# Kernel optimization log

Hardware: AMD Instinct MI355X
Metric: run time of the kernel (lower is better)

## Reference

```python
import jax, jax.numpy as jnp
import numpy as np

B, T, D = 4, 2048, 768
H, HD = 8, 96          # n_heads, head_dim
NB = HD // 24          # number of 24-dim Leech blocks per head
NEG_INF = -1e30


def _leech_kernel_24():
    # QR of the bidiagonal/circulant base matrix, as in generate_leech_kernel
    base = np.zeros((24, 24), dtype=np.float32)
    for i in range(23):
        base[i, i] = 2.0
        base[i, i + 1] = 2.0
    base[23, 23] = 2.0
    base[23, 0] = -2.0
    q, _ = np.linalg.qr(base)
    return jnp.asarray(q, dtype=jnp.float32)


def setup_inputs() -> dict:
    key = jax.random.key(0)
    k1, k2, k3 = jax.random.split(key, 3)
    x = jax.random.normal(k1, (B, T, D), dtype=jnp.float32)
    w_qkv = jax.random.normal(k2, (3 * D, D), dtype=jnp.float32) * (D ** -0.5)
    w_out = jax.random.normal(k3, (D, D), dtype=jnp.float32) * (D ** -0.5)
    kernel = _leech_kernel_24()
    return {"x": x, "w_qkv": w_qkv, "w_out": w_out, "kernel": kernel}


def reference(x, w_qkv, w_out, kernel):
    Bx, Tx, Dx = x.shape
    scale = HD ** -0.5
    # qkv projection (bias=False)
    qkv = jnp.einsum('btd,ed->bte', x, w_qkv)            # [B,T,3D]
    qkv = qkv.reshape(Bx, Tx, 3, H, HD).transpose(2, 0, 3, 1, 4)  # [3,B,H,T,HD]
    q, k, v = qkv[0], qkv[1], qkv[2]
    # per-24-block orthogonal Leech rotation on q and k
    q = jnp.einsum('bhtni,ij->bhtnj', q.reshape(Bx, H, Tx, NB, 24), kernel)
    k = jnp.einsum('bhtni,ij->bhtnj', k.reshape(Bx, H, Tx, NB, 24), kernel)
    q = q.reshape(Bx, H, Tx, HD)
    k = k.reshape(Bx, H, Tx, HD)
    # causal attention (manual softmax; dropout inactive in eval)
    scores = jnp.einsum('bhqd,bhkd->bhqk', q, k) * scale
    causal = jnp.tril(jnp.ones((Tx, Tx), dtype=bool))
    scores = jnp.where(causal[None, None], scores, NEG_INF)
    attn = jax.nn.softmax(scores, axis=-1)
    out = jnp.einsum('bhqk,bhkd->bhqd', attn, v)          # [B,H,T,HD]
    out = out.transpose(0, 2, 1, 3).reshape(Bx, Tx, Dx)
    return jnp.einsum('btd,ed->bte', out, w_out)
```

## Files before the change

kernel.cpp:

```cpp
#include <hip/hip_runtime.h>
#include <cstdint>
#include <cstddef>

#define Bq 4
#define T 2048
#define Dm 768
#define H 8
#define HD 96
#define BH 32
#define QEL ((size_t)BH*T*HD)
#define KEL ((size_t)BH*T*128)
#define PSTRIDE 98304
#define QS 0.14724703336f
#define KVB 64
#define M0 12.0f

typedef unsigned int u32;
typedef unsigned long long u64;
typedef _Float16 f16x8 __attribute__((ext_vector_type(8)));
typedef _Float16 f16x4 __attribute__((ext_vector_type(4)));
typedef float f32x4 __attribute__((ext_vector_type(4)));

__global__ __launch_bounds__(256)
void cvt_fused(const float* __restrict__ x, const float* __restrict__ wq,
               const float* __restrict__ wo, _Float16* __restrict__ xh,
               _Float16* __restrict__ wqh, _Float16* __restrict__ woh)
{
    const int tid  = threadIdx.x;
    const int lane = tid & 63;
    const int gw   = (blockIdx.x * 256 + tid) >> 6;
    const int kc   = gw % 96;
    const int grp  = gw / 96;

    const float* in;
    _Float16* out;
    int row;
    if (grp < 128)      { in = x;  out = xh;  row = grp * 64 + lane; }
    else if (grp < 164) { in = wq; out = wqh; row = (grp - 128) * 64 + lane; }
    else                { in = wo; out = woh; row = (grp - 164) * 64 + lane; }

    const float4 a = *reinterpret_cast<const float4*>(in + (size_t)row * 768 + kc * 8);
    const float4 b = *reinterpret_cast<const float4*>(in + (size_t)row * 768 + kc * 8 + 4);
    f16x8 h;
    h[0] = (_Float16)a.x; h[1] = (_Float16)a.y; h[2] = (_Float16)a.z; h[3] = (_Float16)a.w;
    h[4] = (_Float16)b.x; h[5] = (_Float16)b.y; h[6] = (_Float16)b.z; h[7] = (_Float16)b.w;
    *reinterpret_cast<f16x8*>(
        out + (size_t)(row >> 7) * PSTRIDE + (size_t)kc * 1024 + (row & 127) * 8) = h;
}

template <bool SCATTER>
__global__ __launch_bounds__(256)
void gemm_mfma(const _Float16* __restrict__ At, const _Float16* __restrict__ Bt,
               _Float16* __restrict__ qb, _Float16* __restrict__ kpd,
               _Float16* __restrict__ vtb, float* __restrict__ C,
               int N, int nx)
{
    constexpr int NSTEP = Dm / 32;
    __shared__ _Float16 As[2][4 * 128 * 8];
    __shared__ _Float16 Bs[2][4 * 128 * 8];

    const int tid  = threadIdx.x;
    const int lane = tid & 63;
    const int wid  = tid >> 6;
    const int li   = lane & 15;
    const int lg   = lane >> 4;
    const int wr   = wid >> 1;
    const int wc   = wid & 1;

    const int qch = gridDim.x >> 3;
    const int id  = (blockIdx.x & 7) * qch + (blockIdx.x >> 3);
    const int m0  = (id / nx) * 128;
    const int n0  = (id % nx) * 128;

    const _Float16* baseA = At + (size_t)(m0 >> 7) * PSTRIDE;
    const _Float16* baseB = Bt + (size_t)(n0 >> 7) * PSTRIDE;

    f32x4 acc[4][4];
#pragma unroll
    for (int i = 0; i < 4; ++i)
#pragma unroll
        for (int j = 0; j < 4; ++j) acc[i][j] = (f32x4)0.f;

    auto STAGE = [&](int t, int b) {
        const _Float16* pa = baseA + (t << 12);
        const _Float16* pb = baseB + (t << 12);
#pragma unroll
        for (int i = 0; i < 2; ++i) {
            const int s = wid * 64 + i * 256;
            __builtin_amdgcn_global_load_lds(
                (const __attribute__((address_space(1))) void*)(pa + (size_t)(s + lane) * 8),
                (__attribute__((address_space(3))) void*)&As[b][s * 8], 16, 0, 0);
            __builtin_amdgcn_global_load_lds(
                (const __attribute__((address_space(1))) void*)(pb + (size_t)(s + lane) * 8),
                (__attribute__((address_space(3))) void*)&Bs[b][s * 8], 16, 0, 0);
        }
    };

    STAGE(0, 0);
    for (int t = 0; t < NSTEP; ++t) {
        const int p = t & 1;
        if (t + 1 < NSTEP) {
            STAGE(t + 1, p ^ 1);
            asm volatile("s_waitcnt vmcnt(4)" ::: "memory");
        } else {
            asm volatile("s_waitcnt vmcnt(0)" ::: "memory");
        }
        __builtin_amdgcn_s_barrier();

        f16x8 af[4], bf[4];
#pragma unroll
        for (int i = 0; i < 4; ++i)
            af[i] = *reinterpret_cast<const f16x8*>(
                &As[p][(lg * 128 + wr * 64 + i * 16 + li) * 8]);
#pragma unroll
        for (int j = 0; j < 4; ++j)
            bf[j] = *reinterpret_cast<const f16x8*>(
                &Bs[p][(lg * 128 + wc * 64 + j * 16 + li) * 8]);
#pragma unroll
        for (int i = 0; i < 4; ++i)
#pragma unroll
            for (int j = 0; j < 4; ++j)
                acc[i][j] = __builtin_amdgcn_mfma_f32_16x16x32_f16(
                    af[i], bf[j], acc[i][j], 0, 0, 0);

        asm volatile("s_waitcnt lgkmcnt(0)" ::: "memory");
        __builtin_amdgcn_s_barrier();
    }

#pragma unroll
    for (int i = 0; i < 4; ++i) {
#pragma unroll
        for (int r = 0; r < 4; ++r) {
            const int m = m0 + wr * 64 + i * 16 + lg * 4 + r;
            if (SCATTER) {
                const int b_ = m >> 11, t_ = m & 2047;
#pragma unroll
                for (int j = 0; j < 4; ++j) {
                    const int e = n0 + wc * 64 + j * 16 + li;
                    const int c = e / Dm;
                    const int rem = e - c * Dm;
                    const int h = rem / HD;
                    const int d = rem - h * HD;
                    const size_t bhx = (size_t)(b_ * H + h);
                    const float v = acc[i][j][r];
                    if (c == 0)
                        qb[(bhx * T + t_) * HD + d] = (_Float16)(v * QS);
                    else if (c == 1)
                        kpd[(bhx * T + t_) * 128 + d] = (_Float16)v;
                    else
                        vtb[(bhx * 96 + d) * T + t_] = (_Float16)v;
                }
            } else {
#pragma unroll
                for (int j = 0; j < 4; ++j) {
                    const int n = n0 + wc * 64 + j * 16 + li;
                    C[(size_t)m * N + n] = acc[i][j][r];
                }
            }
        }
    }
}

__global__ __launch_bounds__(256)
void attn_mfma(const _Float16* __restrict__ QG, const _Float16* __restrict__ KG,
               const _Float16* __restrict__ VtG, _Float16* __restrict__ aoh)
{
    __shared__ __align__(16) _Float16 Klds[2][64 * 128];
    __shared__ __align__(16) _Float16 Vlds[2][112 * 64];
    __shared__ __align__(16) _Float16 Pl[4][16][72];

    const int tid  = threadIdx.x;
    const int lane = tid & 63;
    const int wid  = tid >> 6;
    const int lg   = lane >> 4;
    const int li   = lane & 15;

    const int bh = blockIdx.x & 31;
    const int i  = blockIdx.x >> 5;
    const int qt0 = i, qt1 = 31 - i;

    {
        const u32 one2 = 0x3C003C00u;
        u32* vp0 = reinterpret_cast<u32*>(&Vlds[0][96 * 64]);
        u32* vp1 = reinterpret_cast<u32*>(&Vlds[1][96 * 64]);
#pragma unroll
        for (int k = tid; k < 512; k += 256) {
            const u32 v = (k < 32) ? one2 : 0u;
            vp0[k] = v; vp1[k] = v;
        }
    }
    __syncthreads();

    f16x8 qf0[3], qf1[3];
    {
        const _Float16* qr0 = QG + ((size_t)bh * T + qt0 * 64 + wid * 16 + li) * HD;
        const _Float16* qr1 = QG + ((size_t)bh * T + qt1 * 64 + wid * 16 + li) * HD;
#pragma unroll
        for (int ch = 0; ch < 3; ++ch) {
            qf0[ch] = *reinterpret_cast<const f16x8*>(qr0 + ch * 32 + lg * 8);
            qf1[ch] = *reinterpret_cast<const f16x8*>(qr1 + ch * 32 + lg * 8);
        }
    }

    const int swz = (li & 7) << 3;
    int kofs[4][3], vofs[7][2];
#pragma unroll
    for (int kt = 0; kt < 4; ++kt)
#pragma unroll
        for (int ch = 0; ch < 3; ++ch)
            kofs[kt][ch] = (kt * 16 + li) * 128 + ((ch * 32 + lg * 8) ^ swz);
#pragma unroll
    for (int dt = 0; dt < 7; ++dt)
#pragma unroll
        for (int pc = 0; pc < 2; ++pc)
            vofs[dt][pc] = (dt * 16 + li) * 64 + ((pc * 32 + lg * 8) ^ swz);

    const int rK = lane >> 4;
    const int cK = (lane & 15) * 8;
    const int rV = lane >> 3;
    const int cV = (lane & 7) * 8;
    auto STAGE = [&](int kb, int b) {
#pragma unroll
        for (int ii = 0; ii < 4; ++ii) {
            const int r  = wid * 16 + ii * 4 + rK;
            const int c0 = cK ^ (((ii * 4 + rK) & 7) << 3);
            const _Float16* src = KG + ((size_t)(bh * T + kb + r)) * 128 + c0;
            __builtin_amdgcn_global_load_lds(
                (const __attribute__((address_space(1))) void*)src,
                (__attribute__((address_space(3))) void*)&Klds[b][(wid * 16 + ii * 4) * 128],
                16, 0, 0);
        }
#pragma unroll
        for (int jj = 0; jj < 3; ++jj) {
            const int r  = wid * 24 + jj * 8 + rV;
            const int c0 = cV ^ (rV << 3);
            const _Float16* src = VtG + ((size_t)(bh * 96 + r)) * T + kb + c0;
            __builtin_amdgcn_global_load_lds(
                (const __attribute__((address_space(1))) void*)src,
                (__attribute__((address_space(3))) void*)&Vlds[b][(wid * 24 + jj * 8) * 64],
                16, 0, 0);
        }
    };

    f32x4 acc0[7], acc1[7];
#pragma unroll
    for (int dt = 0; dt < 7; ++dt) { acc0[dt] = (f32x4)0.f; acc1[dt] = (f32x4)0.f; }

    auto ROUND_FULL = [&](const f16x8 (&qf)[3], f32x4 (&acc)[7],
                          int p, int nextkb) {
        STAGE(nextkb, p ^ 1);
        asm volatile("s_waitcnt vmcnt(7)" ::: "memory");
        __builtin_amdgcn_s_barrier();

        const _Float16* Kb = &Klds[p][0];
        const _Float16* Vb = &Vlds[p][0];

        f16x8 kf[4][3];
#pragma unroll
        for (int kt = 0; kt < 4; ++kt)
#pragma unroll
            for (int ch = 0; ch < 3; ++ch)
                kf[kt][ch] = *reinterpret_cast<const f16x8*>(Kb + kofs[kt][ch]);

        f32x4 st[4];
        __builtin_amdgcn_s_setprio(1);
#pragma unroll
        for (int kt = 0; kt < 4; ++kt) {
            st[kt] = (f32x4)(-M0);
#pragma unroll
            for (int ch = 0; ch < 3; ++ch)
                st[kt] = __builtin_amdgcn_mfma_f32_16x16x32_f16(
                    kf[kt][ch], qf[ch], st[kt], 0, 0, 0);
        }
        __builtin_amdgcn_s_setprio(0);

#pragma unroll
        for (int kt = 0; kt < 4; ++kt) {
            const auto a = __builtin_amdgcn_cvt_pkrtz(
                __builtin_amdgcn_exp2f(st[kt][0]),
                __builtin_amdgcn_exp2f(st[kt][1]));
            const auto b = __builtin_amdgcn_cvt_pkrtz(
                __builtin_amdgcn_exp2f(st[kt][2]),
                __builtin_amdgcn_exp2f(st[kt][3]));
            const u64 w = (u64)__builtin_bit_cast(u32, a) |
                          ((u64)__builtin_bit_cast(u32, b) << 32);
            *reinterpret_cast<u64*>(&Pl[wid][li][kt * 16 + lg * 4]) = w;
        }

#pragma unroll
        for (int pc = 0; pc < 2; ++pc) {
            const f16x8 pf = *reinterpret_cast<const f16x8*>(
                &Pl[wid][li][pc * 32 + lg * 8]);
            __builtin_amdgcn_s_setprio(1);
#pragma unroll
            for (int dt = 0; dt < 7; ++dt) {
                const f16x8 vf = *reinterpret_cast<const f16x8*>(Vb + vofs[dt][pc]);
                acc[dt] = __builtin_amdgcn_mfma_f32_16x16x32_f16(
                    pf, vf, acc[dt], 0, 0, 0);
            }
            __builtin_amdgcn_s_setprio(0);
        }

        asm volatile("s_waitcnt lgkmcnt(0)" ::: "memory");
        __builtin_amdgcn_s_barrier();
    };

    auto ROUND_DIAG = [&](int kb, int q0w, const f16x8 (&qf)[3], f32x4 (&acc)[7],
                          int p, int nextkb, bool has_next) {
        if (has_next) {
            STAGE(nextkb, p ^ 1);
            asm volatile("s_waitcnt vmcnt(7)" ::: "memory");
        } else {
            asm volatile("s_waitcnt vmcnt(0)" ::: "memory");
        }
        __builtin_amdgcn_s_barrier();

        const _Float16* Kb = &Klds[p][0];
        const _Float16* Vb = &Vlds[p][0];
        const int nkt = min(4, ((q0w + 15 - kb) >> 4) + 1);

        f16x8 kf[4][3];
#pragma unroll
        for (int kt = 0; kt < 4; ++kt)
            if (kt < nkt) {
#pragma unroll
                for (int ch = 0; ch < 3; ++ch)
                    kf[kt][ch] = *reinterpret_cast<const f16x8*>(Kb + kofs[kt][ch]);
            }

        f32x4 st[4];
        __builtin_amdgcn_s_setprio(1);
#pragma unroll
        for (int kt = 0; kt < 4; ++kt) {
            st[kt] = (f32x4)(-M0);
            if (kt < nkt) {
#pragma unroll
                for (int ch = 0; ch < 3; ++ch)
                    st[kt] = __builtin_amdgcn_mfma_f32_16x16x32_f16(
                        kf[kt][ch], qf[ch], st[kt], 0, 0, 0);
            }
        }
        __builtin_amdgcn_s_setprio(0);

        const int qg = q0w + li;
#pragma unroll
        for (int kt = 0; kt < 4; ++kt)
            if (kt < nkt && kb + kt * 16 + 15 > q0w) {
#pragma unroll
                for (int rr = 0; rr < 4; ++rr) {
                    const int kg = kb + kt * 16 + lg * 4 + rr;
                    if (kg > qg) st[kt][rr] = -1e30f;
                }
            }

#pragma unroll
        for (int kt = 0; kt < 4; ++kt)
            if (kt < nkt) {
                const auto a = __builtin_amdgcn_cvt_pkrtz(
                    __builtin_amdgcn_exp2f(st[kt][0]),
                    __builtin_amdgcn_exp2f(st[kt][1]));
                const auto b = __builtin_amdgcn_cvt_pkrtz(
                    __builtin_amdgcn_exp2f(st[kt][2]),
                    __builtin_amdgcn_exp2f(st[kt][3]));
                const u64 w = (u64)__builtin_bit_cast(u32, a) |
                              ((u64)__builtin_bit_cast(u32, b) << 32);
                *reinterpret_cast<u64*>(&Pl[wid][li][kt * 16 + lg * 4]) = w;
            }
        if (nkt & 1)
            *reinterpret_cast<u64*>(&Pl[wid][li][nkt * 16 + lg * 4]) = 0ull;

        const int npc = (nkt + 1) >> 1;
#pragma unroll
        for (int pc = 0; pc < 2; ++pc)
            if (pc < npc) {
                const f16x8 pf = *reinterpret_cast<const f16x8*>(
                    &Pl[wid][li][pc * 32 + lg * 8]);
                __builtin_amdgcn_s_setprio(1);
#pragma unroll
                for (int dt = 0; dt < 7; ++dt) {
                    const f16x8 vf = *reinterpret_cast<const f16x8*>(Vb + vofs[dt][pc]);
                    acc[dt] = __builtin_amdgcn_mfma_f32_16x16x32_f16(
                        pf, vf, acc[dt], 0, 0, 0);
                }
                __builtin_amdgcn_s_setprio(0);
            }

        asm volatile("s_waitcnt lgkmcnt(0)" ::: "memory");
        __builtin_amdgcn_s_barrier();
    };

    STAGE(0, 0);
    const int q0w0 = qt0 * 64 + wid * 16;
    const int q0w1 = qt1 * 64 + wid * 16;
    int r = 0;
    for (int t = 0; t < i; ++t, ++r)
        ROUND_FULL(qf0, acc0, r & 1, (t + 1) * KVB);
    ROUND_DIAG(i * KVB, q0w0, qf0, acc0, r & 1, 0, true); ++r;
    for (int t = 0; t < 31 - i; ++t, ++r)
        ROUND_FULL(qf1, acc1, r & 1, (t + 1) * KVB);
    ROUND_DIAG((31 - i) * KVB, q0w1, qf1, acc1, r & 1, 0, false);

    const int ob = bh >> 3, oh = bh & 7;
#pragma unroll
    for (int rr = 0; rr < 4; ++rr) {
        {
            const float l    = __shfl(acc0[6][rr], lg << 4);
            const float linv = 1.0f / l;
            const int m = ob * T + qt0 * 64 + wid * 16 + lg * 4 + rr;
            _Float16* op = aoh + (size_t)(m >> 7) * PSTRIDE + (size_t)(m & 127) * 8
                         + (size_t)(oh * 12 + (li >> 3)) * 1024 + (li & 7);
#pragma unroll
            for (int dt = 0; dt < 6; ++dt)
                op[dt * 2048] = (_Float16)(acc0[dt][rr] * linv);
        }
        {
            const float l    = __shfl(acc1[6][rr], lg << 4);
            const float linv = 1.0f / l;
            const int m = ob * T + qt1 * 64 + wid * 16 + lg * 4 + rr;
            _Float16* op = aoh + (size_t)(m >> 7) * PSTRIDE + (size_t)(m & 127) * 8
                         + (size_t)(oh * 12 + (li >> 3)) * 1024 + (li & 7);
#pragma unroll
            for (int dt = 0; dt < 6; ++dt)
                op[dt * 2048] = (_Float16)(acc1[dt][rr] * linv);
        }
    }
}

extern "C" void kernel_launch(void* const* d_in, const int* in_sizes, int n_in,
                              void* d_out, int out_size, void* d_ws, size_t ws_size,
                              hipStream_t stream)
{
    const float* x     = (const float*)d_in[0];
    const float* w_qkv = (const float*)d_in[1];
    const float* w_out = (const float*)d_in[2];

    _Float16* qb  = (_Float16*)d_ws;
    _Float16* kpd = qb + QEL;
    _Float16* vtb = kpd + KEL;
    _Float16* aoh = vtb + QEL;
    _Float16* xh  = aoh + (size_t)Bq * T * Dm;
    _Float16* wqh = xh + (size_t)Bq * T * Dm;
    _Float16* woh = wqh + (size_t)3 * Dm * Dm;
    float* out = (float*)d_out;

    const int M = Bq * T;

    cvt_fused<<<dim3((128 + 36 + 12) * 96 / 4), dim3(256), 0, stream>>>(
        x, w_qkv, w_out, xh, wqh, woh);

    gemm_mfma<true><<<dim3((3 * Dm / 128) * (M / 128)), dim3(256), 0, stream>>>(
        xh, wqh, qb, kpd, vtb, nullptr, 3 * Dm, 3 * Dm / 128);

    attn_mfma<<<dim3(BH * (T / 128)), dim3(256), 0, stream>>>(qb, kpd, vtb, aoh);

    gemm_mfma<false><<<dim3((Dm / 128) * (M / 128)), dim3(256), 0, stream>>>(
        aoh, woh, nullptr, nullptr, nullptr, out, Dm, Dm / 128);
}
```

Measured before the change: 149.3 us.

## Split QKV GEMM into dedicated kernel with 256x128 tiles and specialized scatter

Replaces the templated GEMM for the QKV projection with a dedicated kernel that uses a 256x128 output tile per block, so each wave computes a 64x128 strip. The scatter epilogue is specialized per q/k/v section, and the V transpose is written as packed 4-element stores. The aim is more operand reuse per LDS load and fewer index divisions and scattered 2-byte stores. In exchange it uses more accumulator registers, which may lower occupancy, and launches half as many blocks.

Result: slower. 172.3 us (+15.4%).

```diff
diff --git a/kernel.cpp b/kernel.cpp
--- a/kernel.cpp
+++ b/kernel.cpp
@@ -48,12 +48,143 @@
         out + (size_t)(row >> 7) * PSTRIDE + (size_t)kc * 1024 + (row & 127) * 8) = h;
 }
 
-template <bool SCATTER>
 __global__ __launch_bounds__(256)
-void gemm_mfma(const _Float16* __restrict__ At, const _Float16* __restrict__ Bt,
-               _Float16* __restrict__ qb, _Float16* __restrict__ kpd,
-               _Float16* __restrict__ vtb, float* __restrict__ C,
-               int N, int nx)
+void gemm_qkv(const _Float16* __restrict__ At, const _Float16* __restrict__ Bt,
+              _Float16* __restrict__ qb, _Float16* __restrict__ kpd,
+              _Float16* __restrict__ vtb)
+{
+    constexpr int NSTEP = Dm / 32;
+    constexpr int NN = 3 * Dm / 128;
+    __shared__ _Float16 As[2][4 * 256 * 8];
+    __shared__ _Float16 Bs[2][4 * 128 * 8];
+
+    const int tid  = threadIdx.x;
+    const int lane = tid & 63;
+    const int wid  = tid >> 6;
+    const int li   = lane & 15;
+    const int lg   = lane >> 4;
+
+    const int qch = gridDim.x >> 3;
+    const int id  = (blockIdx.x & 7) * qch + (blockIdx.x >> 3);
+    const int m0  = (id / NN) * 256;
+    const int n0  = (id % NN) * 128;
+
+    const _Float16* baseA = At + (size_t)(m0 >> 7) * PSTRIDE;
+    const _Float16* baseB = Bt + (size_t)(n0 >> 7) * PSTRIDE;
+
+    f32x4 acc[4][8];
+#pragma unroll
+    for (int i = 0; i < 4; ++i)
+#pragma unroll
+        for (int j = 0; j < 8; ++j) acc[i][j] = (f32x4)0.f;
+
+    auto STAGE = [&](int t, int b) {
+        const int kofs = (t * 4 + wid) << 10;
+#pragma unroll
+        for (int q = 0; q < 4; ++q) {
+            const _Float16* src = baseA + (q >> 1) * PSTRIDE + kofs
+                                + (size_t)((q & 1) * 64 + lane) * 8;
+            __builtin_amdgcn_global_load_lds(
+                (const __attribute__((address_space(1))) void*)src,
+                (__attribute__((address_space(3))) void*)&As[b][(wid * 256 + q * 64) * 8],
+                16, 0, 0);
+        }
+#pragma unroll
+        for (int q = 0; q < 2; ++q) {
+            const _Float16* src = baseB + kofs + (size_t)(q * 64 + lane) * 8;
+            __builtin_amdgcn_global_load_lds(
+                (const __attribute__((address_space(1))) void*)src,
+                (__attribute__((address_space(3))) void*)&Bs[b][(wid * 128 + q * 64) * 8],
+                16, 0, 0);
+        }
+    };
+
+    STAGE(0, 0);
+    for (int t = 0; t < NSTEP; ++t) {
+        const int p = t & 1;
+        if (t + 1 < NSTEP) {
+            STAGE(t + 1, p ^ 1);
+            asm volatile("s_waitcnt vmcnt(6)" ::: "memory");
+        } else {
+            asm volatile("s_waitcnt vmcnt(0)" ::: "memory");
+        }
+        __builtin_amdgcn_s_barrier();
+
+        f16x8 af[4], bf[8];
+#pragma unroll
+        for (int i = 0; i < 4; ++i)
+            af[i] = *reinterpret_cast<const f16x8*>(
+                &As[p][(lg * 256 + wid * 64 + i * 16 + li) * 8]);
+#pragma unroll
+        for (int j = 0; j < 8; ++j)
+            bf[j] = *reinterpret_cast<const f16x8*>(
+                &Bs[p][(lg * 128 + j * 16 + li) * 8]);
+#pragma unroll
+        for (int i = 0; i < 4; ++i)
+#pragma unroll
+            for (int j = 0; j < 8; ++j)
+                acc[i][j] = __builtin_amdgcn_mfma_f32_16x16x32_f16(
+                    af[i], bf[j], acc[i][j], 0, 0, 0);
+
+        asm volatile("s_waitcnt lgkmcnt(0)" ::: "memory");
+        __builtin_amdgcn_s_barrier();
+    }
+
+    const int c   = n0 / Dm;
+    const int r0  = n0 - c * Dm;
+    const int b_  = m0 >> 11;
+    const int tb0 = (m0 & 2047) + wid * 64;
+
+    if (c == 0) {
+#pragma unroll
+        for (int j = 0; j < 8; ++j) {
+            const int rem = r0 + j * 16 + li;
+            const int h = rem / HD, d = rem - h * HD;
+            const size_t bhx = (size_t)(b_ * H + h);
+#pragma unroll
+            for (int i = 0; i < 4; ++i)
+#pragma unroll
+                for (int r = 0; r < 4; ++r) {
+                    const int t_ = tb0 + i * 16 + lg * 4 + r;
+                    qb[(bhx * T + t_) * HD + d] = (_Float16)(acc[i][j][r] * QS);
+                }
+        }
+    } else if (c == 1) {
+#pragma unroll
+        for (int j = 0; j < 8; ++j) {
+            const int rem = r0 + j * 16 + li;
+            const int h = rem / HD, d = rem - h * HD;
+            const size_t bhx = (size_t)(b_ * H + h);
+#pragma unroll
+            for (int i = 0; i < 4; ++i)
+#pragma unroll
+                for (int r = 0; r < 4; ++r) {
+                    const int t_ = tb0 + i * 16 + lg * 4 + r;
+                    kpd[(bhx * T + t_) * 128 + d] = (_Float16)acc[i][j][r];
+                }
+        }
+    } else {
+#pragma unroll
+        for (int j = 0; j < 8; ++j) {
+            const int rem = r0 + j * 16 + li;
+            const int h = rem / HD, d = rem - h * HD;
+            const size_t bhx = (size_t)(b_ * H + h);
+#pragma unroll
+            for (int i = 0; i < 4; ++i) {
+                const int t_ = tb0 + i * 16 + lg * 4;
+                f16x4 pk;
+                pk[0] = (_Float16)acc[i][j][0]; pk[1] = (_Float16)acc[i][j][1];
+                pk[2] = (_Float16)acc[i][j][2]; pk[3] = (_Float16)acc[i][j][3];
+                *reinterpret_cast<u64*>(&vtb[(bhx * HD + d) * T + t_]) =
+                    __builtin_bit_cast(u64, pk);
+            }
+        }
+    }
+}
+
+__global__ __launch_bounds__(256)
+void gemm_out(const _Float16* __restrict__ At, const _Float16* __restrict__ Bt,
+              float* __restrict__ C, int N, int nx)
 {
     constexpr int NSTEP = Dm / 32;
     __shared__ _Float16 As[2][4 * 128 * 8];
@@ -128,37 +259,16 @@
     }
 
 #pragma unroll
-    for (int i = 0; i < 4; ++i) {
+    for (int i = 0; i < 4; ++i)
 #pragma unroll
         for (int r = 0; r < 4; ++r) {
             const int m = m0 + wr * 64 + i * 16 + lg * 4 + r;
-            if (SCATTER) {
-                const int b_ = m >> 11, t_ = m & 2047;
-#pragma unroll
-                for (int j = 0; j < 4; ++j) {
-                    const int e = n0 + wc * 64 + j * 16 + li;
-                    const int c = e / Dm;
-                    const int rem = e - c * Dm;
-                    const int h = rem / HD;
-                    const int d = rem - h * HD;
-                    const size_t bhx = (size_t)(b_ * H + h);
-                    const float v = acc[i][j][r];
-                    if (c == 0)
-                        qb[(bhx * T + t_) * HD + d] = (_Float16)(v * QS);
-                    else if (c == 1)
-                        kpd[(bhx * T + t_) * 128 + d] = (_Float16)v;
-                    else
-                        vtb[(bhx * 96 + d) * T + t_] = (_Float16)v;
-                }
-            } else {
-#pragma unroll
-                for (int j = 0; j < 4; ++j) {
-                    const int n = n0 + wc * 64 + j * 16 + li;
-                    C[(size_t)m * N + n] = acc[i][j][r];
-                }
-            }
-        }
-    }
+#pragma unroll
+            for (int j = 0; j < 4; ++j) {
+                const int n = n0 + wc * 64 + j * 16 + li;
+                C[(size_t)m * N + n] = acc[i][j][r];
+            }
+        }
 }
 
 __global__ __launch_bounds__(256)
@@ -448,11 +558,11 @@
     cvt_fused<<<dim3((128 + 36 + 12) * 96 / 4), dim3(256), 0, stream>>>(
         x, w_qkv, w_out, xh, wqh, woh);
 
-    gemm_mfma<true><<<dim3((3 * Dm / 128) * (M / 128)), dim3(256), 0, stream>>>(
-        xh, wqh, qb, kpd, vtb, nullptr, 3 * Dm, 3 * Dm / 128);
+    gemm_qkv<<<dim3((M / 256) * (3 * Dm / 128)), dim3(256), 0, stream>>>(
+        xh, wqh, qb, kpd, vtb);
 
     attn_mfma<<<dim3(BH * (T / 128)), dim3(256), 0, stream>>>(qb, kpd, vtb, aoh);
 
-    gemm_mfma<false><<<dim3((Dm / 128) * (M / 128)), dim3(256), 0, stream>>>(
-        aoh, woh, nullptr, nullptr, nullptr, out, Dm, Dm / 128);
+    gemm_out<<<dim3((Dm / 128) * (M / 128)), dim3(256), 0, stream>>>(
+        aoh, woh, out, Dm, Dm / 128);
 }
```
